# Performance work log

Measured on AMD Instinct MI355X. Metric: run time of the kernel, lower is better.

## Reference

```python
import jax, jax.numpy as jnp
import numpy as np

DT = 1.0  # module init dt

def setup_inputs() -> dict:
    key = jax.random.key(0)
    k1, k2 = jax.random.split(key)
    x = jax.random.normal(k1, (8, 4096, 512), dtype=jnp.float32)
    w = jax.random.normal(k2, (512,), dtype=jnp.float32)
    return {"x": x, "w": w}

def reference(x, w):
    # h_t = h_{t-1} + dt*(x_t - relu(w)*h_{t-1}) = a*h_{t-1} + dt*x_t,  a = 1 - dt*relu(w)
    a = (1.0 - DT * jax.nn.relu(w)).astype(x.dtype)  # [d]
    h0 = jnp.zeros((x.shape[0], x.shape[2]), dtype=x.dtype)  # [b, d]
    xt = jnp.swapaxes(x, 0, 1)  # [t, b, d]

    def step(h, x_t):
        h_next = a * h + DT * x_t
        return h_next, h_next

    _, hs = jax.lax.scan(step, h0, xt)  # [t, b, d]
    return jnp.swapaxes(hs, 0, 1)  # [b, t, d] (return_sequences=True)
```

## Files before the change

### kernel.cpp

```cpp
#include <hip/hip_runtime.h>


#define RB 8
#define RT 4096
#define RD 512
#define DG (RD / 4)
#define TC 64
#define NCH (RT / TC)
#define DEPTH 8
#define NOUT (NCH / DEPTH)
#define HB 1e15f

typedef float f32x4 __attribute__((ext_vector_type(4)));

__device__ __forceinline__ float sclamp(float v) {
    return fminf(fmaxf(v, -HB), HB);
}
__device__ __forceinline__ f32x4 sclamp4(f32x4 v) {
    v.x = sclamp(v.x); v.y = sclamp(v.y);
    v.z = sclamp(v.z); v.w = sclamp(v.w);
    return v;
}
__device__ __forceinline__ f32x4 ld4(const float4* __restrict__ p) {
    return *(const f32x4* __restrict__)p;
}
__device__ __forceinline__ f32x4 shfl4(f32x4 v, int src) {
    f32x4 r;
    r.x = __shfl(v.x, src, 64);
    r.y = __shfl(v.y, src, 64);
    r.z = __shfl(v.z, src, 64);
    r.w = __shfl(v.w, src, 64);
    return r;
}

__global__ void __launch_bounds__(256)
rnn_scan(const float4* __restrict__ x4, const float4* __restrict__ w4,
         float4* __restrict__ out4) {
    const int tid   = threadIdx.x;
    const int g     = tid & 3;
    const int wtt   = tid >> 2;
    const int ttl   = wtt & 15;
    const int wv    = tid >> 6;
    const int lanei = tid & 63;

    const int bid  = blockIdx.x;
    const int u    = bid & 7;
    const int half = (bid >> 3) & 1;
    const int rest = bid >> 4;
    const int pair = rest * 8 + u;
    const int b    = pair >> 4;
    const int tile = 2 * (pair & 15) + half;

    const float4 wq = w4[tile * 4 + g];
    f32x4 A1;
    A1.x = 1.0f - fmaxf(wq.x, 0.0f);
    A1.y = 1.0f - fmaxf(wq.y, 0.0f);
    A1.z = 1.0f - fmaxf(wq.z, 0.0f);
    A1.w = 1.0f - fmaxf(wq.w, 0.0f);
    const f32x4 A2  = sclamp4(A1 * A1);
    const f32x4 A4  = sclamp4(A2 * A2);
    const f32x4 A8  = sclamp4(A4 * A4);
    const f32x4 A16 = sclamp4(A8 * A8);

    const int n = ttl + 1;
    f32x4 P = {1.f, 1.f, 1.f, 1.f};
    if (n & 1)  P = sclamp4(P * A1);
    if (n & 2)  P = sclamp4(P * A2);
    if (n & 4)  P = sclamp4(P * A4);
    if (n & 8)  P = sclamp4(P * A8);
    if (n & 16) P = sclamp4(P * A16);

    __shared__ f32x4 Wl[2][4][4];

    const size_t thoff = ((size_t)b * RT + wtt) * DG + (size_t)(tile * 4 + g);
    const float4* __restrict__ xb = x4   + thoff;
    float4*       __restrict__ ob = out4 + thoff;
    const size_t CSTR = (size_t)TC * DG;

    f32x4 pref[DEPTH];
#pragma unroll
    for (int s = 0; s < DEPTH; ++s) pref[s] = ld4(xb + (size_t)s * CSTR);

    f32x4 H = {0.f, 0.f, 0.f, 0.f};

    for (int o = 0; o < NOUT; ++o) {
        f32x4 nxt[DEPTH];
        const bool more = (o + 1 < NOUT);
        if (more) {
#pragma unroll
            for (int s = 0; s < DEPTH; ++s)
                nxt[s] = ld4(xb + (size_t)((o + 1) * DEPTH + s) * CSTR);
        }
#pragma unroll
        for (int s = 0; s < DEPTH; ++s) {
            f32x4 S = pref[s];
            { f32x4 t = shfl4(S, ttl >= 1 ? lanei - 4  : lanei);
              S = (ttl >= 1) ? sclamp4(A1 * t + S) : S; }
            { f32x4 t = shfl4(S, ttl >= 2 ? lanei - 8  : lanei);
              S = (ttl >= 2) ? sclamp4(A2 * t + S) : S; }
            { f32x4 t = shfl4(S, ttl >= 4 ? lanei - 16 : lanei);
              S = (ttl >= 4) ? sclamp4(A4 * t + S) : S; }
            { f32x4 t = shfl4(S, ttl >= 8 ? lanei - 32 : lanei);
              S = (ttl >= 8) ? sclamp4(A8 * t + S) : S; }
            if (ttl == 15) Wl[s & 1][wv][g] = S;
            __syncthreads();
            f32x4 C = H;
            f32x4 Cw = H;
#pragma unroll
            for (int j = 0; j < 4; ++j) {
                if (j == wv) Cw = C;
                C = sclamp4(A16 * C + Wl[s & 1][j][g]);
            }
            H = C;
            f32x4 h = sclamp4(P * Cw + S);
            __builtin_nontemporal_store(
                h, (f32x4*)(ob + (size_t)(o * DEPTH + s) * CSTR));
        }
        if (more) {
#pragma unroll
            for (int s = 0; s < DEPTH; ++s) pref[s] = nxt[s];
        }
    }
}

extern "C" void kernel_launch(void* const* d_in, const int* in_sizes, int n_in,
                              void* d_out, int out_size, void* d_ws, size_t ws_size,
                              hipStream_t stream) {
    const float4* x4 = (const float4*)d_in[0];
    const float4* w4 = (const float4*)d_in[1];
    float4* o4 = (float4*)d_out;
    rnn_scan<<<dim3(RB * (RD / 16)), dim3(256), 0, stream>>>(x4, w4, o4);
}
```

Before: 124.8 us.

## Replace streaming warp-scan with three-phase chunked scan over full sequence per block

Each 1024-thread block now owns the whole 4096-step sequence for 16 channels. Every thread serially scans a 16-step chunk held in registers, a block-wide shuffle scan combines the 256 chunk aggregates through shared memory, and each thread then applies its carry-in to its chunk. This replaces the per-step shuffle scan with a block barrier on every 64-step slice. The aim is to cut shuffle and barrier overhead and keep the data in registers. In exchange each thread does strided 16-row loads with no prefetch overlap, holds many registers at 1024 threads per block, and has fewer blocks in flight to hide memory latency.

```diff
diff --git a/kernel.cpp b/kernel.cpp
--- a/kernel.cpp
+++ b/kernel.cpp
@@ -5,10 +5,9 @@
 #define RT 4096
 #define RD 512
 #define DG (RD / 4)
-#define TC 64
-#define NCH (RT / TC)
-#define DEPTH 8
-#define NOUT (NCH / DEPTH)
+#define CL 16
+#define NC (RT / CL)
+#define TPB 1024
 #define HB 1e15f
 
 typedef float f32x4 __attribute__((ext_vector_type(4)));
@@ -32,16 +31,21 @@
     r.w = __shfl(v.w, src, 64);
     return r;
 }
+__device__ __forceinline__ f32x4 relu_decay(float4 wq) {
+    f32x4 a;
+    a.x = 1.0f - fmaxf(wq.x, 0.0f);
+    a.y = 1.0f - fmaxf(wq.y, 0.0f);
+    a.z = 1.0f - fmaxf(wq.z, 0.0f);
+    a.w = 1.0f - fmaxf(wq.w, 0.0f);
+    return a;
+}
 
-__global__ void __launch_bounds__(256)
-rnn_scan(const float4* __restrict__ x4, const float4* __restrict__ w4,
-         float4* __restrict__ out4) {
-    const int tid   = threadIdx.x;
-    const int g     = tid & 3;
-    const int wtt   = tid >> 2;
-    const int ttl   = wtt & 15;
-    const int wv    = tid >> 6;
-    const int lanei = tid & 63;
+__global__ void __launch_bounds__(TPB)
+rnn_fused(const float4* __restrict__ x4, const float4* __restrict__ w4,
+          float4* __restrict__ out4) {
+    const int tid = threadIdx.x;
+    const int g   = tid & 3;
+    const int c   = tid >> 2;
 
     const int bid  = blockIdx.x;
     const int u    = bid & 7;
@@ -51,74 +55,80 @@
     const int b    = pair >> 4;
     const int tile = 2 * (pair & 15) + half;
 
-    const float4 wq = w4[tile * 4 + g];
-    f32x4 A1;
-    A1.x = 1.0f - fmaxf(wq.x, 0.0f);
-    A1.y = 1.0f - fmaxf(wq.y, 0.0f);
-    A1.z = 1.0f - fmaxf(wq.z, 0.0f);
-    A1.w = 1.0f - fmaxf(wq.w, 0.0f);
-    const f32x4 A2  = sclamp4(A1 * A1);
-    const f32x4 A4  = sclamp4(A2 * A2);
-    const f32x4 A8  = sclamp4(A4 * A4);
-    const f32x4 A16 = sclamp4(A8 * A8);
+    const f32x4 A1 = relu_decay(w4[tile * 4 + g]);
 
-    const int n = ttl + 1;
-    f32x4 P = {1.f, 1.f, 1.f, 1.f};
-    if (n & 1)  P = sclamp4(P * A1);
-    if (n & 2)  P = sclamp4(P * A2);
-    if (n & 4)  P = sclamp4(P * A4);
-    if (n & 8)  P = sclamp4(P * A8);
-    if (n & 16) P = sclamp4(P * A16);
+    __shared__ f32x4 Wagg[NC * 5];
+    __shared__ f32x4 CI[NC * 5];
+    __shared__ f32x4 WinAgg[4 * 5];
 
-    __shared__ f32x4 Wl[2][4][4];
+    const size_t base = ((size_t)b * RT + (size_t)c * CL) * DG
+                      + (size_t)(tile * 4 + g);
+    const float4* __restrict__ xb = x4   + base;
+    float4*       __restrict__ ob = out4 + base;
 
-    const size_t thoff = ((size_t)b * RT + wtt) * DG + (size_t)(tile * 4 + g);
-    const float4* __restrict__ xb = x4   + thoff;
-    float4*       __restrict__ ob = out4 + thoff;
-    const size_t CSTR = (size_t)TC * DG;
+    f32x4 hl[CL];
+#pragma unroll
+    for (int i = 0; i < CL; ++i) hl[i] = ld4(xb + (size_t)i * DG);
+    {
+        f32x4 h = {0.f, 0.f, 0.f, 0.f};
+#pragma unroll
+        for (int i = 0; i < CL; ++i) {
+            h = sclamp4(A1 * h + hl[i]);
+            hl[i] = h;
+        }
+        Wagg[c * 5 + g] = h;
+    }
+    __syncthreads();
 
-    f32x4 pref[DEPTH];
+    {
+        const int w  = tid >> 6;
+        const int l  = tid & 63;
+        const int g2 = w & 3;
+        const int q  = w >> 2;
+        const int cc = q * 64 + l;
+
+        f32x4 B = relu_decay(w4[tile * 4 + g2]);
 #pragma unroll
-    for (int s = 0; s < DEPTH; ++s) pref[s] = ld4(xb + (size_t)s * CSTR);
+        for (int i = 0; i < 4; ++i) B = sclamp4(B * B);
 
-    f32x4 H = {0.f, 0.f, 0.f, 0.f};
+        f32x4 S = Wagg[cc * 5 + g2];
+        f32x4 M = B;
+#pragma unroll
+        for (int s = 1; s < 64; s <<= 1) {
+            f32x4 t = shfl4(S, l >= s ? l - s : l);
+            S = (l >= s) ? sclamp4(M * t + S) : S;
+            M = sclamp4(M * M);
+        }
+        if (l == 63) WinAgg[q * 5 + g2] = S;
+        __syncthreads();
 
-    for (int o = 0; o < NOUT; ++o) {
-        f32x4 nxt[DEPTH];
-        const bool more = (o + 1 < NOUT);
-        if (more) {
+        f32x4 WC = {0.f, 0.f, 0.f, 0.f};
 #pragma unroll
-            for (int s = 0; s < DEPTH; ++s)
-                nxt[s] = ld4(xb + (size_t)((o + 1) * DEPTH + s) * CSTR);
+        for (int j = 0; j < 3; ++j) {
+            if (j < q) WC = sclamp4(M * WC + WinAgg[j * 5 + g2]);
         }
+        const int n = l + 1;
+        f32x4 P = {1.f, 1.f, 1.f, 1.f};
+        f32x4 mm = B;
 #pragma unroll
-        for (int s = 0; s < DEPTH; ++s) {
-            f32x4 S = pref[s];
-            { f32x4 t = shfl4(S, ttl >= 1 ? lanei - 4  : lanei);
-              S = (ttl >= 1) ? sclamp4(A1 * t + S) : S; }
-            { f32x4 t = shfl4(S, ttl >= 2 ? lanei - 8  : lanei);
-              S = (ttl >= 2) ? sclamp4(A2 * t + S) : S; }
-            { f32x4 t = shfl4(S, ttl >= 4 ? lanei - 16 : lanei);
-              S = (ttl >= 4) ? sclamp4(A4 * t + S) : S; }
-            { f32x4 t = shfl4(S, ttl >= 8 ? lanei - 32 : lanei);
-              S = (ttl >= 8) ? sclamp4(A8 * t + S) : S; }
-            if (ttl == 15) Wl[s & 1][wv][g] = S;
-            __syncthreads();
-            f32x4 C = H;
-            f32x4 Cw = H;
+        for (int k = 0; k < 7; ++k) {
+            if ((n >> k) & 1) P = sclamp4(P * mm);
+            mm = sclamp4(mm * mm);
+        }
+        f32x4 Sf = sclamp4(S + P * WC);
+        if (cc < NC - 1) CI[(cc + 1) * 5 + g2] = Sf;
+        if (cc == 0)     CI[0 * 5 + g2] = (f32x4){0.f, 0.f, 0.f, 0.f};
+    }
+    __syncthreads();
+
+    {
+        const f32x4 C = CI[c * 5 + g];
+        f32x4 p = A1;
 #pragma unroll
-            for (int j = 0; j < 4; ++j) {
-                if (j == wv) Cw = C;
-                C = sclamp4(A16 * C + Wl[s & 1][j][g]);
-            }
-            H = C;
-            f32x4 h = sclamp4(P * Cw + S);
-            __builtin_nontemporal_store(
-                h, (f32x4*)(ob + (size_t)(o * DEPTH + s) * CSTR));
-        }
-        if (more) {
-#pragma unroll
-            for (int s = 0; s < DEPTH; ++s) pref[s] = nxt[s];
+        for (int i = 0; i < CL; ++i) {
+            f32x4 o = sclamp4(hl[i] + p * C);
+            __builtin_nontemporal_store(o, (f32x4*)(ob + (size_t)i * DG));
+            p = sclamp4(p * A1);
         }
     }
 }
@@ -129,5 +139,5 @@
     const float4* x4 = (const float4*)d_in[0];
     const float4* w4 = (const float4*)d_in[1];
     float4* o4 = (float4*)d_out;
-    rnn_scan<<<dim3(RB * (RD / 16)), dim3(256), 0, stream>>>(x4, w4, o4);
+    rnn_fused<<<dim3(RB * (RD / 16)), dim3(TPB), 0, stream>>>(x4, w4, o4);
 }
```

Measured after the change: 123.6 us. No clear change (-1.0%).
